# Performance work log

Hardware: AMD Instinct MI355X
Metric: run time of the kernel (lower is better)

## Reference

```python
import jax, jax.numpy as jnp
import numpy as np

N_NODES = 100000
N_EDGES = 3200000
IN_DIM = 256
HID_DIM = 64
OUT_DIM = 64


def setup_inputs() -> dict:
    key = jax.random.key(0)
    k1, k2, k3, k4, k5, k6 = jax.random.split(key, 6)
    x = jax.random.normal(k1, (N_NODES, IN_DIM), dtype=jnp.float32)
    edge_index = jax.random.randint(k2, (2, N_EDGES), 0, N_NODES, dtype=jnp.int32)
    # Glorot-style init for the two GCNConv layers (PyG default: glorot weight, zero bias)
    W1 = jax.random.normal(k3, (IN_DIM, HID_DIM), dtype=jnp.float32) * (1.0 / np.sqrt(IN_DIM))
    b1 = jnp.zeros((HID_DIM,), dtype=jnp.float32)
    W2 = jax.random.normal(k4, (HID_DIM, OUT_DIM), dtype=jnp.float32) * (1.0 / np.sqrt(HID_DIM))
    b2 = jnp.zeros((OUT_DIM,), dtype=jnp.float32)
    return {"x": x, "edge_index": edge_index, "W1": W1, "b1": b1, "W2": W2, "b2": b2}


def _gcn_conv(x, src, dst, deg_inv_sqrt, W, b, n):
    # PyG GCNConv: h = x W; out_i = sum_j norm_ij * h_j + b, with symmetric norm
    h = x @ W                                   # (n, d_out) small GEMM
    norm = deg_inv_sqrt[src] * deg_inv_sqrt[dst]  # (E+n,)
    msg = norm[:, None] * h[src]                # gather (E+n, d_out)
    agg = jax.ops.segment_sum(msg, dst, num_segments=n)  # scatter-add
    return agg + b


def reference(x, edge_index, W1, b1, W2, b2):
    n = x.shape[0]
    loops = jnp.arange(n, dtype=edge_index.dtype)
    src = jnp.concatenate([edge_index[0], loops])
    dst = jnp.concatenate([edge_index[1], loops])
    # degree on destination (col) with added self-loops, weight 1.0
    deg = jax.ops.segment_sum(jnp.ones_like(dst, dtype=x.dtype), dst, num_segments=n)
    deg_inv_sqrt = jnp.where(deg > 0, jax.lax.rsqrt(deg), 0.0)
    h = jax.nn.relu(_gcn_conv(x, src, dst, deg_inv_sqrt, W1, b1, n))
    return _gcn_conv(h, src, dst, deg_inv_sqrt, W2, b2, n)
```

## Files before the change

### kernel.cpp

```cpp
#include <hip/hip_runtime.h>
#include <cstdint>
#include <cstddef>


#define BIN_SHIFT 7
#define BIN_NODES 128
#define MAX_BINS 1024
#define SRC_BITS 17
#define SRC_MASK ((1 << SRC_BITS) - 1)

typedef unsigned short ushort_t;

__device__ __forceinline__ float4 bfq2f4(uint2 p) {
  float4 r;
  r.x = __uint_as_float(p.x << 16);
  r.y = __uint_as_float(p.x & 0xFFFF0000u);
  r.z = __uint_as_float(p.y << 16);
  r.w = __uint_as_float(p.y & 0xFFFF0000u);
  return r;
}
__device__ __forceinline__ unsigned f2bf(float f) {
  unsigned u = __float_as_uint(f);
  return (u + 0x7FFFu + ((u >> 16) & 1u)) >> 16;
}
__device__ __forceinline__ uint2 f42bfq(float4 f) {
  uint2 r;
  r.x = f2bf(f.x) | (f2bf(f.y) << 16);
  r.y = f2bf(f.z) | (f2bf(f.w) << 16);
  return r;
}

__global__ void zero_int(int* __restrict__ p, int n) {
  int i = blockIdx.x * blockDim.x + threadIdx.x;
  if (i < n) p[i] = 0;
}

__global__ __launch_bounds__(256) void bin_count(const int* __restrict__ dst, int E, int nbins,
                                                 int* __restrict__ binCnt) {
  __shared__ int h[MAX_BINS];
  for (int i = threadIdx.x; i < nbins; i += 256) h[i] = 0;
  __syncthreads();
  int stride = gridDim.x * 256;
  for (int e = blockIdx.x * 256 + threadIdx.x; e < E; e += stride)
    atomicAdd(&h[dst[e] >> BIN_SHIFT], 1);
  __syncthreads();
  for (int i = threadIdx.x; i < nbins; i += 256)
    if (h[i]) atomicAdd(&binCnt[i], h[i]);
}

__global__ __launch_bounds__(256) void bin_scan(const int* __restrict__ binCnt, int nbins, int E,
                                                int* __restrict__ binStart,
                                                int* __restrict__ binCursor) {
  __shared__ int s[256];
  int t = threadIdx.x;
  int c[4];
  int sum = 0;
#pragma unroll
  for (int i = 0; i < 4; i++) {
    int idx = t * 4 + i;
    c[i] = (idx < nbins) ? binCnt[idx] : 0;
    sum += c[i];
  }
  int v = sum;
  s[t] = v;
  __syncthreads();
  for (int d = 1; d < 256; d <<= 1) {
    int add = (t >= d) ? s[t - d] : 0;
    __syncthreads();
    s[t] += add;
    __syncthreads();
  }
  int run = s[t] - v;
#pragma unroll
  for (int i = 0; i < 4; i++) {
    int idx = t * 4 + i;
    if (idx < nbins) {
      binStart[idx] = run;
      binCursor[idx] = run;
      run += c[i];
    }
  }
  if (t == 0) binStart[nbins] = E;
}

__global__ __launch_bounds__(256) void bin_fill(const int* __restrict__ src,
                                                const int* __restrict__ dst, int E, int nbins,
                                                int* __restrict__ binCursor,
                                                unsigned* __restrict__ binbuf) {
  __shared__ int h[MAX_BINS];
  __shared__ int lbase[MAX_BINS];
  __shared__ int lcnt[MAX_BINS];
  int chunk = (E + gridDim.x - 1) / gridDim.x;
  int c0 = blockIdx.x * chunk;
  int c1 = min(E, c0 + chunk);
  for (int i = threadIdx.x; i < nbins; i += 256) {
    h[i] = 0;
    lcnt[i] = 0;
  }
  __syncthreads();
  for (int e = c0 + threadIdx.x; e < c1; e += 256) atomicAdd(&h[dst[e] >> BIN_SHIFT], 1);
  __syncthreads();
  for (int i = threadIdx.x; i < nbins; i += 256)
    lbase[i] = h[i] ? atomicAdd(&binCursor[i], h[i]) : 0;
  __syncthreads();
  for (int e = c0 + threadIdx.x; e < c1; e += 256) {
    int d = dst[e];
    int b = d >> BIN_SHIFT;
    int idx = lbase[b] + atomicAdd(&lcnt[b], 1);
    binbuf[idx] = ((unsigned)(d & (BIN_NODES - 1)) << SRC_BITS) | (unsigned)src[e];
  }
}

__global__ __launch_bounds__(256) void node_count_dis(const unsigned* __restrict__ binbuf,
                                                      const int* __restrict__ binStart, int N,
                                                      int* __restrict__ count,
                                                      float* __restrict__ dis) {
  __shared__ int cnt[BIN_NODES];
  int b = blockIdx.x;
  int nodeBase = b << BIN_SHIFT;
  if (threadIdx.x < BIN_NODES) cnt[threadIdx.x] = 0;
  __syncthreads();
  int s0 = binStart[b], s1 = binStart[b + 1];
  for (int i = s0 + threadIdx.x; i < s1; i += 256) atomicAdd(&cnt[binbuf[i] >> SRC_BITS], 1);
  __syncthreads();
  if (threadIdx.x < BIN_NODES) {
    int node = nodeBase + threadIdx.x;
    if (node < N) {
      int c = cnt[threadIdx.x];
      count[node] = c;
      dis[node] = rsqrtf((float)(c + 1));
    }
  }
}

__global__ void scan_partial(const int* __restrict__ count, int* __restrict__ bsum, int N) {
  __shared__ int s[256];
  int t = threadIdx.x, b = blockIdx.x;
  int base = b * 1024 + t * 4;
  int sum = 0;
#pragma unroll
  for (int i = 0; i < 4; i++) sum += (base + i < N) ? count[base + i] : 0;
  s[t] = sum;
  __syncthreads();
  for (int d = 128; d > 0; d >>= 1) {
    if (t < d) s[t] += s[t + d];
    __syncthreads();
  }
  if (t == 0) bsum[b] = s[0];
}

__global__ void scan_blocksums(int* __restrict__ bsum, int nb) {
  __shared__ int s[256];
  int t = threadIdx.x;
  int v = (t < nb) ? bsum[t] : 0;
  s[t] = v;
  __syncthreads();
  for (int d = 1; d < 256; d <<= 1) {
    int add = (t >= d) ? s[t - d] : 0;
    __syncthreads();
    s[t] += add;
    __syncthreads();
  }
  if (t < nb) bsum[t] = s[t] - v;
}

__global__ void scan_final(const int* __restrict__ count, const int* __restrict__ bsum,
                           int* __restrict__ rowptr, int N, int E) {
  __shared__ int s[256];
  int t = threadIdx.x, b = blockIdx.x;
  int base = b * 1024 + t * 4;
  int c[4];
  int sum = 0;
#pragma unroll
  for (int i = 0; i < 4; i++) {
    c[i] = (base + i < N) ? count[base + i] : 0;
    sum += c[i];
  }
  int v = sum;
  s[t] = v;
  __syncthreads();
  for (int d = 1; d < 256; d <<= 1) {
    int add = (t >= d) ? s[t - d] : 0;
    __syncthreads();
    s[t] += add;
    __syncthreads();
  }
  int run = bsum[b] + (s[t] - v);
#pragma unroll
  for (int i = 0; i < 4; i++) {
    if (base + i < N) {
      rowptr[base + i] = run;
      run += c[i];
    }
  }
  if (b == 0 && t == 0) rowptr[N] = E;
}

__global__ __launch_bounds__(256) void csr_fill(const unsigned* __restrict__ binbuf,
                                                const int* __restrict__ binStart,
                                                const int* __restrict__ rowptr,
                                                const float* __restrict__ dis, int N,
                                                int* __restrict__ col, float* __restrict__ wgt) {
  __shared__ int cur[BIN_NODES];
  __shared__ float dloc[BIN_NODES];
  int b = blockIdx.x;
  int nodeBase = b << BIN_SHIFT;
  if (threadIdx.x < BIN_NODES) {
    int node = nodeBase + threadIdx.x;
    cur[threadIdx.x] = (node < N) ? rowptr[node] : 0;
    dloc[threadIdx.x] = (node < N) ? dis[node] : 0.f;
  }
  __syncthreads();
  int s0 = binStart[b], s1 = binStart[b + 1];
  for (int i = s0 + threadIdx.x; i < s1; i += 256) {
    unsigned e = binbuf[i];
    int dl = e >> SRC_BITS;
    int sidx = e & SRC_MASK;
    int slot = atomicAdd(&cur[dl], 1);
    col[slot] = sidx;
    wgt[slot] = dis[sidx] * dloc[dl];
  }
}

template <int K, bool ABF16>
__global__ __launch_bounds__(256, 4) void gemm64(const void* __restrict__ Av,
                                                 const float* __restrict__ W,
                                                 uint2* __restrict__ Cb, int M) {
  constexpr int CHUNK = (K > 128) ? 128 : K;
  __shared__ float4 wlds[CHUNK * 16];

  const int c0 = threadIdx.x & 15;
  const int rq = threadIdx.x >> 4;
  const int r0 = blockIdx.x * 64 + rq * 4;

  float4 acc[4];
#pragma unroll
  for (int i = 0; i < 4; i++) acc[i] = make_float4(0.f, 0.f, 0.f, 0.f);
  size_t aoff[4];
  bool ok[4];
#pragma unroll
  for (int i = 0; i < 4; i++) {
    int r = r0 + i;
    ok[i] = (r < M);
    aoff[i] = (size_t)(ok[i] ? r : (M - 1)) * K;
  }

  for (int kc = 0; kc < K; kc += CHUNK) {
    {
      const float4* W4 = (const float4*)W + (size_t)kc * 16;
      for (int i = threadIdx.x; i < CHUNK * 16; i += 256) wlds[i] = W4[i];
    }
    __syncthreads();

#pragma unroll 2
    for (int k = 0; k < CHUNK; k += 4) {
      float4 xv[4];
#pragma unroll
      for (int i = 0; i < 4; i++) {
        size_t idx = aoff[i] + kc + k;
        if (ABF16)
          xv[i] = bfq2f4(*(const uint2*)((const ushort_t*)Av + idx));
        else
          xv[i] = *(const float4*)((const float*)Av + idx);
      }
      float4 w0 = wlds[(k + 0) * 16 + c0];
      float4 w1 = wlds[(k + 1) * 16 + c0];
      float4 w2 = wlds[(k + 2) * 16 + c0];
      float4 w3 = wlds[(k + 3) * 16 + c0];
#pragma unroll
      for (int i = 0; i < 4; i++) {
        acc[i].x += xv[i].x * w0.x + xv[i].y * w1.x + xv[i].z * w2.x + xv[i].w * w3.x;
        acc[i].y += xv[i].x * w0.y + xv[i].y * w1.y + xv[i].z * w2.y + xv[i].w * w3.y;
        acc[i].z += xv[i].x * w0.z + xv[i].y * w1.z + xv[i].z * w2.z + xv[i].w * w3.z;
        acc[i].w += xv[i].x * w0.w + xv[i].y * w1.w + xv[i].z * w2.w + xv[i].w * w3.w;
      }
    }
    __syncthreads();
  }
#pragma unroll
  for (int i = 0; i < 4; i++)
    if (ok[i]) Cb[(size_t)(r0 + i) * 16 + c0] = f42bfq(acc[i]);
}

template <bool OUTBF>
__global__ __launch_bounds__(256) void agg_kernel(
    const uint2* __restrict__ h, const int* __restrict__ rowptr, const int* __restrict__ col,
    const float* __restrict__ wgt, const float* __restrict__ dis, const float* __restrict__ bias,
    void* __restrict__ outv, int N, int relu) {
  int wid = (blockIdx.x * blockDim.x + threadIdx.x) >> 6;
  if (wid >= N) return;
  int lane = threadIdx.x & 63;
  int sub = lane & 15;
  int quarter = lane >> 4;

  int start = rowptr[wid], end = rowptr[wid + 1];
  float di = dis[wid];

  float4 a0 = make_float4(0.f, 0.f, 0.f, 0.f), a1 = a0, a2 = a0, a3 = a0;
  {
    float4 self = bfq2f4(h[(size_t)wid * 16 + sub]);
    if (quarter == 0) {
      a0.x = di * di * self.x;
      a0.y = di * di * self.y;
      a0.z = di * di * self.z;
      a0.w = di * di * self.w;
    }
  }

  for (int base = start; base < end; base += 64) {
    int e = base + lane;
    int sj = 0;
    float wj = 0.f;
    if (e < end) {
      sj = col[e];
      wj = wgt[e];
    }
    int cnt = end - base;
    if (cnt > 64) cnt = 64;
    int rounds = (cnt + 3) >> 2;
    int t = 0;
    for (; t + 4 <= rounds; t += 4) {
      int i0 = 4 * t + quarter;
      int s0 = __shfl(sj, i0), s1 = __shfl(sj, i0 + 4), s2 = __shfl(sj, i0 + 8),
          s3 = __shfl(sj, i0 + 12);
      float w0 = __shfl(wj, i0), w1 = __shfl(wj, i0 + 4), w2 = __shfl(wj, i0 + 8),
            w3 = __shfl(wj, i0 + 12);
      float4 g0 = bfq2f4(h[(size_t)s0 * 16 + sub]);
      float4 g1 = bfq2f4(h[(size_t)s1 * 16 + sub]);
      float4 g2 = bfq2f4(h[(size_t)s2 * 16 + sub]);
      float4 g3 = bfq2f4(h[(size_t)s3 * 16 + sub]);
      a0.x += w0 * g0.x; a0.y += w0 * g0.y; a0.z += w0 * g0.z; a0.w += w0 * g0.w;
      a1.x += w1 * g1.x; a1.y += w1 * g1.y; a1.z += w1 * g1.z; a1.w += w1 * g1.w;
      a2.x += w2 * g2.x; a2.y += w2 * g2.y; a2.z += w2 * g2.z; a2.w += w2 * g2.w;
      a3.x += w3 * g3.x; a3.y += w3 * g3.y; a3.z += w3 * g3.z; a3.w += w3 * g3.w;
    }
    for (; t < rounds; t++) {
      int i0 = 4 * t + quarter;
      int s0 = __shfl(sj, i0);
      float w0 = __shfl(wj, i0);
      float4 g0 = bfq2f4(h[(size_t)s0 * 16 + sub]);
      a0.x += w0 * g0.x; a0.y += w0 * g0.y; a0.z += w0 * g0.z; a0.w += w0 * g0.w;
    }
  }

  float sx = (a0.x + a1.x) + (a2.x + a3.x);
  float sy = (a0.y + a1.y) + (a2.y + a3.y);
  float sz = (a0.z + a1.z) + (a2.z + a3.z);
  float sw = (a0.w + a1.w) + (a2.w + a3.w);
  sx += __shfl_down(sx, 32); sy += __shfl_down(sy, 32);
  sz += __shfl_down(sz, 32); sw += __shfl_down(sw, 32);
  sx += __shfl_down(sx, 16); sy += __shfl_down(sy, 16);
  sz += __shfl_down(sz, 16); sw += __shfl_down(sw, 16);
  if (quarter == 0) {
    float4 bv = ((const float4*)bias)[sub];
    float4 o = make_float4(sx + bv.x, sy + bv.y, sz + bv.z, sw + bv.w);
    if (relu) {
      o.x = fmaxf(o.x, 0.f);
      o.y = fmaxf(o.y, 0.f);
      o.z = fmaxf(o.z, 0.f);
      o.w = fmaxf(o.w, 0.f);
    }
    if (OUTBF)
      ((uint2*)outv)[(size_t)wid * 16 + sub] = f42bfq(o);
    else
      ((float4*)outv)[(size_t)wid * 16 + sub] = o;
  }
}

extern "C" void kernel_launch(void* const* d_in, const int* in_sizes, int n_in,
                              void* d_out, int out_size, void* d_ws, size_t ws_size,
                              hipStream_t stream) {
  const float* x = (const float*)d_in[0];
  const int* ei = (const int*)d_in[1];
  const float* W1 = (const float*)d_in[2];
  const float* b1 = (const float*)d_in[3];
  const float* W2 = (const float*)d_in[4];
  const float* b2 = (const float*)d_in[5];

  const int IN = 256;
  const int E = in_sizes[1] / 2;
  const int N = in_sizes[0] / IN;
  const int* src = ei;
  const int* dst = ei + E;
  const int nbins = (N + BIN_NODES - 1) >> BIN_SHIFT;

  char* ws = (char*)d_ws;
  size_t off = 0;
  auto alloc = [&](size_t bytes) -> void* {
    void* p = ws + off;
    off += (bytes + 255) & ~(size_t)255;
    return p;
  };
  int* count = (int*)alloc((size_t)N * 4);
  int* rowptr = (int*)alloc((size_t)(N + 1) * 4);
  float* dis = (float*)alloc((size_t)N * 4);
  int* bsum = (int*)alloc(4096);
  int* binCnt = (int*)alloc(MAX_BINS * 4);
  int* binStart = (int*)alloc((MAX_BINS + 1) * 4);
  int* binCursor = (int*)alloc(MAX_BINS * 4);
  int* col = (int*)alloc((size_t)E * 4);
  float* wgt = (float*)alloc((size_t)E * 4);
  uint2* out1 = (uint2*)alloc((size_t)N * 64 * 2);
  size_t big = ((size_t)E * 4 > (size_t)N * 128) ? (size_t)E * 4 : (size_t)N * 128;
  unsigned* binbuf = (unsigned*)alloc(big);
  uint2* h = (uint2*)binbuf;
  float* outf = (float*)d_out;

  const int tb = 256;
  const int nb = (N + 1023) / 1024;

  zero_int<<<(nbins + tb - 1) / tb, tb, 0, stream>>>(binCnt, nbins);
  bin_count<<<1024, 256, 0, stream>>>(dst, E, nbins, binCnt);
  bin_scan<<<1, 256, 0, stream>>>(binCnt, nbins, E, binStart, binCursor);
  bin_fill<<<512, 256, 0, stream>>>(src, dst, E, nbins, binCursor, binbuf);
  node_count_dis<<<nbins, 256, 0, stream>>>(binbuf, binStart, N, count, dis);
  scan_partial<<<nb, 256, 0, stream>>>(count, bsum, N);
  scan_blocksums<<<1, 256, 0, stream>>>(bsum, nb);
  scan_final<<<nb, 256, 0, stream>>>(count, bsum, rowptr, N, E);
  csr_fill<<<nbins, 256, 0, stream>>>(binbuf, binStart, rowptr, dis, N, col, wgt);

  gemm64<256, false><<<(N + 63) / 64, 256, 0, stream>>>(x, W1, h, N);
  agg_kernel<true><<<(N + 3) / 4, 256, 0, stream>>>(h, rowptr, col, wgt, dis, b1, out1, N, 1);
  gemm64<64, true><<<(N + 63) / 64, 256, 0, stream>>>(out1, W2, h, N);
  agg_kernel<false><<<(N + 3) / 4, 256, 0, stream>>>(h, rowptr, col, wgt, dis, b2, outf, N, 0);
}
```

Before: 540.6 us.

## Two-level binning for CSR build, fused rowptr scan, drop per-edge weight array

Measured after the change: 508.1 us. -6.0%, faster.

```diff
diff --git a/kernel.cpp b/kernel.cpp
--- a/kernel.cpp
+++ b/kernel.cpp
@@ -6,6 +6,10 @@
 #define BIN_SHIFT 7
 #define BIN_NODES 128
 #define MAX_BINS 1024
+#define SUP_SHIFT 11
+#define FINE_PER_SUP 16
+#define NSUP_MAX 64
+#define SCAP 56
 #define SRC_BITS 17
 #define SRC_MASK ((1 << SRC_BITS) - 1)
 
@@ -50,7 +54,8 @@
 
 __global__ __launch_bounds__(256) void bin_scan(const int* __restrict__ binCnt, int nbins, int E,
                                                 int* __restrict__ binStart,
-                                                int* __restrict__ binCursor) {
+                                                int* __restrict__ binCursor,
+                                                int* __restrict__ supCursor) {
   __shared__ int s[256];
   int t = threadIdx.x;
   int c[4];
@@ -77,37 +82,99 @@
     if (idx < nbins) {
       binStart[idx] = run;
       binCursor[idx] = run;
+      if ((idx & (FINE_PER_SUP - 1)) == 0) supCursor[idx >> 4] = run;
       run += c[i];
     }
   }
   if (t == 0) binStart[nbins] = E;
 }
 
-__global__ __launch_bounds__(256) void bin_fill(const int* __restrict__ src,
-                                                const int* __restrict__ dst, int E, int nbins,
-                                                int* __restrict__ binCursor,
-                                                unsigned* __restrict__ binbuf) {
-  __shared__ int h[MAX_BINS];
-  __shared__ int lbase[MAX_BINS];
-  __shared__ int lcnt[MAX_BINS];
+__global__ __launch_bounds__(256) void super_fill(const int* __restrict__ src,
+                                                  const int* __restrict__ dst, int E, int nsup,
+                                                  int* __restrict__ supCursor,
+                                                  unsigned* __restrict__ supbuf) {
+  __shared__ unsigned stage[NSUP_MAX * SCAP];
+  __shared__ int lcnt[NSUP_MAX], lbase[NSUP_MAX], lscan[NSUP_MAX + 1];
   int chunk = (E + gridDim.x - 1) / gridDim.x;
   int c0 = blockIdx.x * chunk;
   int c1 = min(E, c0 + chunk);
-  for (int i = threadIdx.x; i < nbins; i += 256) {
-    h[i] = 0;
-    lcnt[i] = 0;
-  }
-  __syncthreads();
-  for (int e = c0 + threadIdx.x; e < c1; e += 256) atomicAdd(&h[dst[e] >> BIN_SHIFT], 1);
-  __syncthreads();
-  for (int i = threadIdx.x; i < nbins; i += 256)
-    lbase[i] = h[i] ? atomicAdd(&binCursor[i], h[i]) : 0;
-  __syncthreads();
-  for (int e = c0 + threadIdx.x; e < c1; e += 256) {
-    int d = dst[e];
-    int b = d >> BIN_SHIFT;
-    int idx = lbase[b] + atomicAdd(&lcnt[b], 1);
-    binbuf[idx] = ((unsigned)(d & (BIN_NODES - 1)) << SRC_BITS) | (unsigned)src[e];
+  for (int t0 = c0; t0 < c1; t0 += 2048) {
+    int t1 = min(c1, t0 + 2048);
+    if (threadIdx.x < nsup) lcnt[threadIdx.x] = 0;
+    __syncthreads();
+    for (int e = t0 + threadIdx.x; e < t1; e += 256) {
+      int d = dst[e];
+      int sb = d >> SUP_SHIFT;
+      unsigned v = ((unsigned)(d & ((1 << SUP_SHIFT) - 1)) << SRC_BITS) | (unsigned)src[e];
+      int idx = atomicAdd(&lcnt[sb], 1);
+      if (idx < SCAP)
+        stage[sb * SCAP + idx] = v;
+      else {
+        int g = atomicAdd(&supCursor[sb], 1);
+        supbuf[g] = v;
+      }
+    }
+    __syncthreads();
+    if (threadIdx.x < nsup) {
+      int c = min(lcnt[threadIdx.x], SCAP);
+      lcnt[threadIdx.x] = c;
+      lbase[threadIdx.x] = c ? atomicAdd(&supCursor[threadIdx.x], c) : 0;
+    }
+    __syncthreads();
+    if (threadIdx.x == 0) {
+      int r = 0;
+      for (int i = 0; i < nsup; i++) {
+        lscan[i] = r;
+        r += lcnt[i];
+      }
+      lscan[nsup] = r;
+    }
+    __syncthreads();
+    int total = lscan[nsup];
+    for (int j = threadIdx.x; j < total; j += 256) {
+      int lo = 0, hi = nsup;
+      while (hi - lo > 1) {
+        int mid = (lo + hi) >> 1;
+        if (lscan[mid] <= j)
+          lo = mid;
+        else
+          hi = mid;
+      }
+      int off = j - lscan[lo];
+      supbuf[lbase[lo] + off] = stage[lo * SCAP + off];
+    }
+    __syncthreads();
+  }
+}
+
+__global__ __launch_bounds__(256) void fine_fill(const unsigned* __restrict__ supbuf,
+                                                 const int* __restrict__ binStart, int nbins,
+                                                 int* __restrict__ binCursor,
+                                                 unsigned* __restrict__ binbuf) {
+  __shared__ int lcnt[FINE_PER_SUP], lbase[FINE_PER_SUP];
+  int sb = blockIdx.x >> 3, p = blockIdx.x & 7;
+  int seg0 = binStart[sb << 4];
+  int seg1 = binStart[min((sb + 1) << 4, nbins)];
+  int part = (seg1 - seg0 + 7) >> 3;
+  int c0 = seg0 + p * part;
+  int c1 = min(seg1, c0 + part);
+  if (threadIdx.x < FINE_PER_SUP) lcnt[threadIdx.x] = 0;
+  __syncthreads();
+  for (int i = c0 + threadIdx.x; i < c1; i += 256) atomicAdd(&lcnt[supbuf[i] >> 24], 1);
+  __syncthreads();
+  if (threadIdx.x < FINE_PER_SUP) {
+    int c = lcnt[threadIdx.x];
+    lbase[threadIdx.x] = c ? atomicAdd(&binCursor[(sb << 4) + threadIdx.x], c) : 0;
+    lcnt[threadIdx.x] = 0;
+  }
+  __syncthreads();
+  for (int i = c0 + threadIdx.x; i < c1; i += 256) {
+    unsigned v = supbuf[i];
+    unsigned dls = v >> SRC_BITS;
+    int f = dls >> BIN_SHIFT;
+    unsigned vf = ((dls & (BIN_NODES - 1)) << SRC_BITS) | (v & SRC_MASK);
+    int idx = lbase[f] + atomicAdd(&lcnt[f], 1);
+    binbuf[idx] = vf;
   }
 }
 
@@ -133,92 +200,43 @@
   }
 }
 
-__global__ void scan_partial(const int* __restrict__ count, int* __restrict__ bsum, int N) {
-  __shared__ int s[256];
-  int t = threadIdx.x, b = blockIdx.x;
-  int base = b * 1024 + t * 4;
-  int sum = 0;
-#pragma unroll
-  for (int i = 0; i < 4; i++) sum += (base + i < N) ? count[base + i] : 0;
-  s[t] = sum;
-  __syncthreads();
-  for (int d = 128; d > 0; d >>= 1) {
-    if (t < d) s[t] += s[t + d];
-    __syncthreads();
-  }
-  if (t == 0) bsum[b] = s[0];
-}
-
-__global__ void scan_blocksums(int* __restrict__ bsum, int nb) {
-  __shared__ int s[256];
-  int t = threadIdx.x;
-  int v = (t < nb) ? bsum[t] : 0;
-  s[t] = v;
-  __syncthreads();
-  for (int d = 1; d < 256; d <<= 1) {
-    int add = (t >= d) ? s[t - d] : 0;
-    __syncthreads();
-    s[t] += add;
-    __syncthreads();
-  }
-  if (t < nb) bsum[t] = s[t] - v;
-}
-
-__global__ void scan_final(const int* __restrict__ count, const int* __restrict__ bsum,
-                           int* __restrict__ rowptr, int N, int E) {
-  __shared__ int s[256];
-  int t = threadIdx.x, b = blockIdx.x;
-  int base = b * 1024 + t * 4;
-  int c[4];
-  int sum = 0;
-#pragma unroll
-  for (int i = 0; i < 4; i++) {
-    c[i] = (base + i < N) ? count[base + i] : 0;
-    sum += c[i];
-  }
-  int v = sum;
-  s[t] = v;
-  __syncthreads();
-  for (int d = 1; d < 256; d <<= 1) {
-    int add = (t >= d) ? s[t - d] : 0;
-    __syncthreads();
-    s[t] += add;
-    __syncthreads();
-  }
-  int run = bsum[b] + (s[t] - v);
-#pragma unroll
-  for (int i = 0; i < 4; i++) {
-    if (base + i < N) {
-      rowptr[base + i] = run;
-      run += c[i];
-    }
-  }
-  if (b == 0 && t == 0) rowptr[N] = E;
-}
-
-__global__ __launch_bounds__(256) void csr_fill(const unsigned* __restrict__ binbuf,
-                                                const int* __restrict__ binStart,
-                                                const int* __restrict__ rowptr,
-                                                const float* __restrict__ dis, int N,
-                                                int* __restrict__ col, float* __restrict__ wgt) {
+__global__ __launch_bounds__(256) void bin_csr(const unsigned* __restrict__ binbuf,
+                                               const int* __restrict__ binStart,
+                                               const int* __restrict__ count, int N, int E,
+                                               int* __restrict__ rowptr, int* __restrict__ col) {
   __shared__ int cur[BIN_NODES];
-  __shared__ float dloc[BIN_NODES];
-  int b = blockIdx.x;
+  __shared__ int pref[BIN_NODES];
+  int b = blockIdx.x, t = threadIdx.x;
   int nodeBase = b << BIN_SHIFT;
-  if (threadIdx.x < BIN_NODES) {
-    int node = nodeBase + threadIdx.x;
-    cur[threadIdx.x] = (node < N) ? rowptr[node] : 0;
-    dloc[threadIdx.x] = (node < N) ? dis[node] : 0.f;
-  }
-  __syncthreads();
-  int s0 = binStart[b], s1 = binStart[b + 1];
-  for (int i = s0 + threadIdx.x; i < s1; i += 256) {
-    unsigned e = binbuf[i];
-    int dl = e >> SRC_BITS;
-    int sidx = e & SRC_MASK;
-    int slot = atomicAdd(&cur[dl], 1);
-    col[slot] = sidx;
-    wgt[slot] = dis[sidx] * dloc[dl];
+  int c = 0;
+  if (t < BIN_NODES) {
+    int node = nodeBase + t;
+    c = (node < N) ? count[node] : 0;
+    pref[t] = c;
+  }
+  __syncthreads();
+  for (int d = 1; d < BIN_NODES; d <<= 1) {
+    int add = (t < BIN_NODES && t >= d) ? pref[t - d] : 0;
+    __syncthreads();
+    if (t < BIN_NODES) pref[t] += add;
+    __syncthreads();
+  }
+  int s0 = binStart[b];
+  if (t < BIN_NODES) {
+    int node = nodeBase + t;
+    if (node < N) {
+      int ex = s0 + pref[t] - c;
+      rowptr[node] = ex;
+      cur[t] = ex;
+    }
+  }
+  if (b == 0 && t == 255) rowptr[N] = E;
+  __syncthreads();
+  int s1 = binStart[b + 1];
+  for (int i = s0 + t; i < s1; i += 256) {
+    unsigned v = binbuf[i];
+    int slot = atomicAdd(&cur[v >> SRC_BITS], 1);
+    col[slot] = v & SRC_MASK;
   }
 }
 
@@ -285,8 +303,8 @@
 template <bool OUTBF>
 __global__ __launch_bounds__(256) void agg_kernel(
     const uint2* __restrict__ h, const int* __restrict__ rowptr, const int* __restrict__ col,
-    const float* __restrict__ wgt, const float* __restrict__ dis, const float* __restrict__ bias,
-    void* __restrict__ outv, int N, int relu) {
+    const float* __restrict__ dis, const float* __restrict__ bias, void* __restrict__ outv,
+    int N, int relu) {
   int wid = (blockIdx.x * blockDim.x + threadIdx.x) >> 6;
   if (wid >= N) return;
   int lane = threadIdx.x & 63;
@@ -300,10 +318,10 @@
   {
     float4 self = bfq2f4(h[(size_t)wid * 16 + sub]);
     if (quarter == 0) {
-      a0.x = di * di * self.x;
-      a0.y = di * di * self.y;
-      a0.z = di * di * self.z;
-      a0.w = di * di * self.w;
+      a0.x = di * self.x;
+      a0.y = di * self.y;
+      a0.z = di * self.z;
+      a0.w = di * self.w;
     }
   }
 
@@ -313,7 +331,7 @@
     float wj = 0.f;
     if (e < end) {
       sj = col[e];
-      wj = wgt[e];
+      wj = dis[sj];
     }
     int cnt = end - base;
     if (cnt > 64) cnt = 64;
@@ -353,7 +371,7 @@
   sz += __shfl_down(sz, 16); sw += __shfl_down(sw, 16);
   if (quarter == 0) {
     float4 bv = ((const float4*)bias)[sub];
-    float4 o = make_float4(sx + bv.x, sy + bv.y, sz + bv.z, sw + bv.w);
+    float4 o = make_float4(di * sx + bv.x, di * sy + bv.y, di * sz + bv.z, di * sw + bv.w);
     if (relu) {
       o.x = fmaxf(o.x, 0.f);
       o.y = fmaxf(o.y, 0.f);
@@ -383,6 +401,7 @@
   const int* src = ei;
   const int* dst = ei + E;
   const int nbins = (N + BIN_NODES - 1) >> BIN_SHIFT;
+  const int nsup = (N + (1 << SUP_SHIFT) - 1) >> SUP_SHIFT;
 
   char* ws = (char*)d_ws;
   size_t off = 0;
@@ -394,33 +413,28 @@
   int* count = (int*)alloc((size_t)N * 4);
   int* rowptr = (int*)alloc((size_t)(N + 1) * 4);
   float* dis = (float*)alloc((size_t)N * 4);
-  int* bsum = (int*)alloc(4096);
   int* binCnt = (int*)alloc(MAX_BINS * 4);
   int* binStart = (int*)alloc((MAX_BINS + 1) * 4);
   int* binCursor = (int*)alloc(MAX_BINS * 4);
+  int* supCursor = (int*)alloc(NSUP_MAX * 4);
   int* col = (int*)alloc((size_t)E * 4);
-  float* wgt = (float*)alloc((size_t)E * 4);
+  unsigned* supbuf = (unsigned*)col;
   uint2* out1 = (uint2*)alloc((size_t)N * 64 * 2);
   size_t big = ((size_t)E * 4 > (size_t)N * 128) ? (size_t)E * 4 : (size_t)N * 128;
   unsigned* binbuf = (unsigned*)alloc(big);
   uint2* h = (uint2*)binbuf;
   float* outf = (float*)d_out;
 
-  const int tb = 256;
-  const int nb = (N + 1023) / 1024;
-
-  zero_int<<<(nbins + tb - 1) / tb, tb, 0, stream>>>(binCnt, nbins);
+  zero_int<<<(nbins + 255) / 256, 256, 0, stream>>>(binCnt, nbins);
   bin_count<<<1024, 256, 0, stream>>>(dst, E, nbins, binCnt);
-  bin_scan<<<1, 256, 0, stream>>>(binCnt, nbins, E, binStart, binCursor);
-  bin_fill<<<512, 256, 0, stream>>>(src, dst, E, nbins, binCursor, binbuf);
+  bin_scan<<<1, 256, 0, stream>>>(binCnt, nbins, E, binStart, binCursor, supCursor);
+  super_fill<<<512, 256, 0, stream>>>(src, dst, E, nsup, supCursor, supbuf);
+  fine_fill<<<nsup * 8, 256, 0, stream>>>(supbuf, binStart, nbins, binCursor, binbuf);
   node_count_dis<<<nbins, 256, 0, stream>>>(binbuf, binStart, N, count, dis);
-  scan_partial<<<nb, 256, 0, stream>>>(count, bsum, N);
-  scan_blocksums<<<1, 256, 0, stream>>>(bsum, nb);
-  scan_final<<<nb, 256, 0, stream>>>(count, bsum, rowptr, N, E);
-  csr_fill<<<nbins, 256, 0, stream>>>(binbuf, binStart, rowptr, dis, N, col, wgt);
+  bin_csr<<<nbins, 256, 0, stream>>>(binbuf, binStart, count, N, E, rowptr, col);
 
   gemm64<256, false><<<(N + 63) / 64, 256, 0, stream>>>(x, W1, h, N);
-  agg_kernel<true><<<(N + 3) / 4, 256, 0, stream>>>(h, rowptr, col, wgt, dis, b1, out1, N, 1);
+  agg_kernel<true><<<(N + 3) / 4, 256, 0, stream>>>(h, rowptr, col, dis, b1, out1, N, 1);
   gemm64<64, true><<<(N + 63) / 64, 256, 0, stream>>>(out1, W2, h, N);
-  agg_kernel<false><<<(N + 3) / 4, 256, 0, stream>>>(h, rowptr, col, wgt, dis, b2, outf, N, 0);
-}
+  agg_kernel<false><<<(N + 3) / 4, 256, 0, stream>>>(h, rowptr, col, dis, b2, outf, N, 0);
+}
```
